# Optimization experiments

Measured on AMD Instinct MI355X. Metric: run time of the kernel, lower is better.

Reference implementation:

```python
import jax, jax.numpy as jnp
import numpy as np

E = 500000
NODE_DIM = 128
EDGE_DIM = 64
OUT_DIM = 128
LN_EPS = 1e-5  # torch nn.LayerNorm default


def setup_inputs() -> dict:
    key = jax.random.key(0)
    ks = jax.random.split(key, 8)
    in_dim = NODE_DIM + EDGE_DIM
    # kaiming-uniform-ish init scale like torch Linear default
    b1 = 1.0 / np.sqrt(in_dim)
    b2 = 1.0 / np.sqrt(OUT_DIM)
    return {
        "source_features": jax.random.normal(ks[0], (E, NODE_DIM), dtype=jnp.float32),
        "edge_features": jax.random.normal(ks[1], (E, EDGE_DIM), dtype=jnp.float32),
        "W1": jax.random.uniform(ks[2], (in_dim, OUT_DIM), jnp.float32, -b1, b1),
        "b1": jax.random.uniform(ks[3], (OUT_DIM,), jnp.float32, -b1, b1),
        "ln_gamma": jnp.ones((OUT_DIM,), jnp.float32),
        "ln_beta": jnp.zeros((OUT_DIM,), jnp.float32),
        "W2": jax.random.uniform(ks[4], (OUT_DIM, OUT_DIM), jnp.float32, -b2, b2),
        "b2": jax.random.uniform(ks[5], (OUT_DIM,), jnp.float32, -b2, b2),
    }


def reference(source_features, edge_features, W1, b1, ln_gamma, ln_beta, W2, b2):
    # Concat source-node and edge features: (E, node_dim + edge_dim)
    x = jnp.concatenate([source_features, edge_features], axis=-1)
    # Linear 1: (E, out_dim)
    h = x @ W1 + b1
    # LayerNorm over last dim (eps matches torch default)
    mu = jnp.mean(h, axis=-1, keepdims=True)
    var = jnp.mean(jnp.square(h - mu), axis=-1, keepdims=True)
    h = (h - mu) * jax.lax.rsqrt(var + LN_EPS) * ln_gamma + ln_beta
    # SiLU -> Linear 2 -> SiLU
    h = jax.nn.silu(h)
    h = h @ W2 + b2
    return jax.nn.silu(h)
```

## Files before the change

### kernel.cpp

```cpp
#include <hip/hip_runtime.h>
#include <stdint.h>

#define E_TOTAL   500000
#define NODE_DIM  128
#define EDGE_DIM  64
#define IN_DIM    192
#define OUT_DIM_  128
#define LN_EPS    1e-5f
#define NTILES    ((E_TOTAL + 63) / 64)

typedef __attribute__((ext_vector_type(8))) short  short8;
typedef __attribute__((ext_vector_type(4))) float  floatx4;
typedef __attribute__((ext_vector_type(4))) unsigned int uintx4;

union Frag { short8 s; uintx4 u; };

__device__ __forceinline__ unsigned int cvtpk(float a, float b) {
    unsigned int r;
    asm("v_cvt_pk_bf16_f32 %0, %1, %2" : "=v"(r) : "v"(a), "v"(b));
    return r;
}
__device__ __forceinline__ unsigned short f2bf1(float a) {
    unsigned int r;
    asm("v_cvt_pk_bf16_f32 %0, %1, %1" : "=v"(r) : "v"(a));
    return (unsigned short)r;
}
__device__ __forceinline__ float fexp2(float x) {
    float r; asm("v_exp_f32 %0, %1" : "=v"(r) : "v"(x)); return r;
}
__device__ __forceinline__ float frcp(float x) {
    float r; asm("v_rcp_f32 %0, %1" : "=v"(r) : "v"(x)); return r;
}
__device__ __forceinline__ float frsq(float x) {
    float r; asm("v_rsq_f32 %0, %1" : "=v"(r) : "v"(x)); return r;
}
__device__ __forceinline__ float silu(float y) {
    return y * frcp(1.0f + fexp2(y * -1.44269504f));
}

__launch_bounds__(256, 2)
__global__ void edge_mlp_kernel(
    const float* __restrict__ src,
    const float* __restrict__ edg,
    const float* __restrict__ W1,
    const float* __restrict__ b1,
    const float* __restrict__ gam,
    const float* __restrict__ bet,
    const float* __restrict__ W2,
    const float* __restrict__ b2,
    float* __restrict__ out)
{
    __shared__ uintx4 w1f[48 * 64];
    __shared__ __align__(16) float ws[4][1088];
    __shared__ float pl[512];

    const int tid  = threadIdx.x;
    const int lane = tid & 63;
    const int wave = tid >> 6;
    const int quad = lane >> 4;
    const int l15  = lane & 15;

    #pragma unroll
    for (int i = 0; i < 12; ++i) {
        int f = wave + 4 * i;
        int s = f >> 3, t = f & 7;
        const float* wp = W1 + (size_t)(s * 32 + quad * 8) * OUT_DIM_ + t * 16 + l15;
        uintx4 v;
        v.x = cvtpk(wp[0],            wp[OUT_DIM_]);
        v.y = cvtpk(wp[2 * OUT_DIM_], wp[3 * OUT_DIM_]);
        v.z = cvtpk(wp[4 * OUT_DIM_], wp[5 * OUT_DIM_]);
        v.w = cvtpk(wp[6 * OUT_DIM_], wp[7 * OUT_DIM_]);
        w1f[f * 64 + lane] = v;
    }
    pl[tid]       = (tid < 128) ? b1[tid]  : gam[tid - 128];
    pl[256 + tid] = (tid < 128) ? bet[tid] : b2[tid - 128];

    Frag w2r[32];
    #pragma unroll
    for (int f = 0; f < 32; ++f) {
        int s = f >> 3, t = f & 7;
        const float* wp = W2 + (size_t)(s * 32 + quad * 8) * OUT_DIM_ + t * 16 + l15;
        w2r[f].u.x = cvtpk(wp[0],            wp[OUT_DIM_]);
        w2r[f].u.y = cvtpk(wp[2 * OUT_DIM_], wp[3 * OUT_DIM_]);
        w2r[f].u.z = cvtpk(wp[4 * OUT_DIM_], wp[5 * OUT_DIM_]);
        w2r[f].u.w = cvtpk(wp[6 * OUT_DIM_], wp[7 * OUT_DIM_]);
    }
    __syncthreads();

    unsigned short* hst = (unsigned short*)&ws[wave][0];
    float*          ost = &ws[wave][0];

    int tile = blockIdx.x;
    floatx4 nx[12];
    {
        int r = tile * 64 + wave * 16 + l15;
        int rc = r < E_TOTAL ? r : (E_TOTAL - 1);
        const float* sp = src + (size_t)rc * NODE_DIM + quad * 8;
        const float* ep = edg + (size_t)rc * EDGE_DIM + quad * 8;
        #pragma unroll
        for (int s = 0; s < 4; ++s) {
            nx[2 * s]     = *(const floatx4*)(sp + s * 32);
            nx[2 * s + 1] = *(const floatx4*)(sp + s * 32 + 4);
        }
        #pragma unroll
        for (int s = 0; s < 2; ++s) {
            nx[8 + 2 * s] = *(const floatx4*)(ep + s * 32);
            nx[9 + 2 * s] = *(const floatx4*)(ep + s * 32 + 4);
        }
    }

    for (; tile < NTILES; tile += gridDim.x) {
        const int rbase = tile * 64 + wave * 16;

        floatx4 acc[8];
        #pragma unroll
        for (int t = 0; t < 8; ++t) {
            float bb = pl[t * 16 + l15];
            acc[t] = (floatx4)(bb);
        }

        #pragma unroll
        for (int s = 0; s < 6; ++s) {
            floatx4 x0 = nx[2 * s];
            floatx4 x1 = nx[2 * s + 1];
            Frag a;
            a.u.x = cvtpk(x0.x, x0.y);
            a.u.y = cvtpk(x0.z, x0.w);
            a.u.z = cvtpk(x1.x, x1.y);
            a.u.w = cvtpk(x1.z, x1.w);
            #pragma unroll
            for (int t = 0; t < 8; ++t) {
                Frag w; w.u = w1f[(s * 8 + t) * 64 + lane];
                acc[t] = __builtin_amdgcn_mfma_f32_16x16x32_bf16(a.s, w.s, acc[t], 0, 0, 0);
            }
        }

        {
            int tn = tile + gridDim.x;
            if (tn < NTILES) {
                int r = tn * 64 + wave * 16 + l15;
                int rc = r < E_TOTAL ? r : (E_TOTAL - 1);
                const float* sp = src + (size_t)rc * NODE_DIM + quad * 8;
                const float* ep = edg + (size_t)rc * EDGE_DIM + quad * 8;
                #pragma unroll
                for (int s = 0; s < 4; ++s) {
                    nx[2 * s]     = *(const floatx4*)(sp + s * 32);
                    nx[2 * s + 1] = *(const floatx4*)(sp + s * 32 + 4);
                }
                #pragma unroll
                for (int s = 0; s < 2; ++s) {
                    nx[8 + 2 * s] = *(const floatx4*)(ep + s * 32);
                    nx[9 + 2 * s] = *(const floatx4*)(ep + s * 32 + 4);
                }
            }
        }

        float S1[4] = {0, 0, 0, 0}, S2[4] = {0, 0, 0, 0};
        #pragma unroll
        for (int t = 0; t < 8; ++t) {
            #pragma unroll
            for (int j = 0; j < 4; ++j) {
                float h = acc[t][j];
                S1[j] += h;
                S2[j] += h * h;
            }
        }
        #pragma unroll
        for (int m = 1; m < 16; m <<= 1) {
            #pragma unroll
            for (int j = 0; j < 4; ++j) {
                S1[j] += __shfl_xor(S1[j], m, 64);
                S2[j] += __shfl_xor(S2[j], m, 64);
            }
        }
        float mu[4], rs[4];
        #pragma unroll
        for (int j = 0; j < 4; ++j) {
            mu[j] = S1[j] * (1.0f / 128.0f);
            float var = S2[j] * (1.0f / 128.0f) - mu[j] * mu[j];
            rs[j] = frsq(var + LN_EPS);
        }

        #pragma unroll
        for (int t = 0; t < 8; ++t) {
            float g  = pl[128 + t * 16 + l15];
            float bt = pl[256 + t * 16 + l15];
            #pragma unroll
            for (int j = 0; j < 4; ++j) {
                float gs  = rs[j] * g;
                float off = __builtin_fmaf(-mu[j], gs, bt);
                float y   = __builtin_fmaf(acc[t][j], gs, off);
                hst[(quad * 4 + j) * 136 + t * 16 + l15] = f2bf1(silu(y));
            }
        }

        #pragma unroll
        for (int t = 0; t < 8; ++t) {
            float bb2 = pl[384 + t * 16 + l15];
            acc[t] = (floatx4)(bb2);
        }
        #pragma unroll
        for (int s2 = 0; s2 < 4; ++s2) {
            Frag a2;
            a2.u = *(const uintx4*)&hst[l15 * 136 + s2 * 32 + quad * 8];
            #pragma unroll
            for (int t = 0; t < 8; ++t) {
                acc[t] = __builtin_amdgcn_mfma_f32_16x16x32_bf16(a2.s, w2r[s2 * 8 + t].s, acc[t], 0, 0, 0);
            }
        }

        #pragma unroll
        for (int p = 0; p < 2; ++p) {
            #pragma unroll
            for (int t = 0; t < 8; ++t) {
                #pragma unroll
                for (int jj = 0; jj < 2; ++jj) {
                    float y = acc[t][2 * p + jj];
                    ost[(quad * 2 + jj) * 136 + t * 16 + l15] = silu(y);
                }
            }
            {
                int a = lane >> 3;
                int b = lane & 7;
                int grow = rbase + (a >> 1) * 4 + 2 * p + (a & 1);
                if (grow < E_TOTAL) {
                    const float* rp = ost + a * 136 + b * 4;
                    float* op = out + (size_t)grow * OUT_DIM_ + b * 4;
                    #pragma unroll
                    for (int c = 0; c < 4; ++c) {
                        *(floatx4*)(op + 32 * c) = *(const floatx4*)(rp + 32 * c);
                    }
                }
            }
        }
    }
}

extern "C" void kernel_launch(void* const* d_in, const int* in_sizes, int n_in,
                              void* d_out, int out_size, void* d_ws, size_t ws_size,
                              hipStream_t stream) {
    const float* src = (const float*)d_in[0];
    const float* edg = (const float*)d_in[1];
    const float* W1  = (const float*)d_in[2];
    const float* b1  = (const float*)d_in[3];
    const float* gam = (const float*)d_in[4];
    const float* bet = (const float*)d_in[5];
    const float* W2  = (const float*)d_in[6];
    const float* b2  = (const float*)d_in[7];
    float* out = (float*)d_out;

    edge_mlp_kernel<<<512, 256, 0, stream>>>(src, edg, W1, b1, gam, bet, W2, b2, out);
}
```

Before: 518.0 us.

## Swap MFMA operands so rows lie in columns, simplifying LayerNorm and staging

Both MFMAs now take the weights as the A operand and the activations as B, so each lane holds four consecutive output features of a single edge row. LayerNorm statistics then need only two cross-quad shuffles per row instead of four shuffle rounds on four values. The normalized hidden values and outputs are written to LDS as 128-bit packed vectors rather than scalar shorts and floats. W2 register fragments are re-permuted to match the new K ordering of the hidden staging, and the output staging uses a 68-float row stride in two 64-column halves, trading a more intricate index mapping for fewer LDS and shuffle instructions.

```diff
diff --git a/kernel.cpp b/kernel.cpp
--- a/kernel.cpp
+++ b/kernel.cpp
@@ -19,11 +19,6 @@
     unsigned int r;
     asm("v_cvt_pk_bf16_f32 %0, %1, %2" : "=v"(r) : "v"(a), "v"(b));
     return r;
-}
-__device__ __forceinline__ unsigned short f2bf1(float a) {
-    unsigned int r;
-    asm("v_cvt_pk_bf16_f32 %0, %1, %1" : "=v"(r) : "v"(a));
-    return (unsigned short)r;
 }
 __device__ __forceinline__ float fexp2(float x) {
     float r; asm("v_exp_f32 %0, %1" : "=v"(r) : "v"(x)); return r;
@@ -59,6 +54,7 @@
     const int wave = tid >> 6;
     const int quad = lane >> 4;
     const int l15  = lane & 15;
+    const int q4   = quad * 4;
 
     #pragma unroll
     for (int i = 0; i < 12; ++i) {
@@ -78,12 +74,12 @@
     Frag w2r[32];
     #pragma unroll
     for (int f = 0; f < 32; ++f) {
-        int s = f >> 3, t = f & 7;
-        const float* wp = W2 + (size_t)(s * 32 + quad * 8) * OUT_DIM_ + t * 16 + l15;
-        w2r[f].u.x = cvtpk(wp[0],            wp[OUT_DIM_]);
-        w2r[f].u.y = cvtpk(wp[2 * OUT_DIM_], wp[3 * OUT_DIM_]);
-        w2r[f].u.z = cvtpk(wp[4 * OUT_DIM_], wp[5 * OUT_DIM_]);
-        w2r[f].u.w = cvtpk(wp[6 * OUT_DIM_], wp[7 * OUT_DIM_]);
+        int s2 = f >> 3, t = f & 7;
+        const float* wp = W2 + (size_t)(32 * quad + 4 * s2) * OUT_DIM_ + t * 16 + l15;
+        w2r[f].u.x = cvtpk(wp[0],              wp[OUT_DIM_]);
+        w2r[f].u.y = cvtpk(wp[2 * OUT_DIM_],   wp[3 * OUT_DIM_]);
+        w2r[f].u.z = cvtpk(wp[16 * OUT_DIM_],  wp[17 * OUT_DIM_]);
+        w2r[f].u.w = cvtpk(wp[18 * OUT_DIM_],  wp[19 * OUT_DIM_]);
     }
     __syncthreads();
 
@@ -114,10 +110,8 @@
 
         floatx4 acc[8];
         #pragma unroll
-        for (int t = 0; t < 8; ++t) {
-            float bb = pl[t * 16 + l15];
-            acc[t] = (floatx4)(bb);
-        }
+        for (int t = 0; t < 8; ++t)
+            acc[t] = *(const floatx4*)&pl[t * 16 + q4];
 
         #pragma unroll
         for (int s = 0; s < 6; ++s) {
@@ -131,7 +125,7 @@
             #pragma unroll
             for (int t = 0; t < 8; ++t) {
                 Frag w; w.u = w1f[(s * 8 + t) * 64 + lane];
-                acc[t] = __builtin_amdgcn_mfma_f32_16x16x32_bf16(a.s, w.s, acc[t], 0, 0, 0);
+                acc[t] = __builtin_amdgcn_mfma_f32_16x16x32_bf16(w.s, a.s, acc[t], 0, 0, 0);
             }
         }
 
@@ -155,81 +149,89 @@
             }
         }
 
-        float S1[4] = {0, 0, 0, 0}, S2[4] = {0, 0, 0, 0};
+        float S1 = 0.0f, S2 = 0.0f;
         #pragma unroll
         for (int t = 0; t < 8; ++t) {
             #pragma unroll
             for (int j = 0; j < 4; ++j) {
                 float h = acc[t][j];
-                S1[j] += h;
-                S2[j] += h * h;
-            }
-        }
-        #pragma unroll
-        for (int m = 1; m < 16; m <<= 1) {
-            #pragma unroll
-            for (int j = 0; j < 4; ++j) {
-                S1[j] += __shfl_xor(S1[j], m, 64);
-                S2[j] += __shfl_xor(S2[j], m, 64);
-            }
-        }
-        float mu[4], rs[4];
-        #pragma unroll
-        for (int j = 0; j < 4; ++j) {
-            mu[j] = S1[j] * (1.0f / 128.0f);
-            float var = S2[j] * (1.0f / 128.0f) - mu[j] * mu[j];
-            rs[j] = frsq(var + LN_EPS);
-        }
-
-        #pragma unroll
-        for (int t = 0; t < 8; ++t) {
-            float g  = pl[128 + t * 16 + l15];
-            float bt = pl[256 + t * 16 + l15];
-            #pragma unroll
-            for (int j = 0; j < 4; ++j) {
-                float gs  = rs[j] * g;
-                float off = __builtin_fmaf(-mu[j], gs, bt);
-                float y   = __builtin_fmaf(acc[t][j], gs, off);
-                hst[(quad * 4 + j) * 136 + t * 16 + l15] = f2bf1(silu(y));
-            }
-        }
-
-        #pragma unroll
-        for (int t = 0; t < 8; ++t) {
-            float bb2 = pl[384 + t * 16 + l15];
-            acc[t] = (floatx4)(bb2);
-        }
+                S1 += h;
+                S2 += h * h;
+            }
+        }
+        S1 += __shfl_xor(S1, 16, 64);
+        S2 += __shfl_xor(S2, 16, 64);
+        S1 += __shfl_xor(S1, 32, 64);
+        S2 += __shfl_xor(S2, 32, 64);
+        float mu = S1 * (1.0f / 128.0f);
+        float var = S2 * (1.0f / 128.0f) - mu * mu;
+        float rs = frsq(var + LN_EPS);
+
+        #pragma unroll
+        for (int u = 0; u < 4; ++u) {
+            uintx4 d;
+            #pragma unroll
+            for (int h2 = 0; h2 < 2; ++h2) {
+                int t = 2 * u + h2;
+                floatx4 g4 = *(const floatx4*)&pl[128 + t * 16 + q4];
+                floatx4 bt4 = *(const floatx4*)&pl[256 + t * 16 + q4];
+                float y0, y1, y2, y3;
+                {
+                    float gs = rs * g4.x;
+                    y0 = silu(__builtin_fmaf(acc[t][0], gs, __builtin_fmaf(-mu, gs, bt4.x)));
+                }
+                {
+                    float gs = rs * g4.y;
+                    y1 = silu(__builtin_fmaf(acc[t][1], gs, __builtin_fmaf(-mu, gs, bt4.y)));
+                }
+                {
+                    float gs = rs * g4.z;
+                    y2 = silu(__builtin_fmaf(acc[t][2], gs, __builtin_fmaf(-mu, gs, bt4.z)));
+                }
+                {
+                    float gs = rs * g4.w;
+                    y3 = silu(__builtin_fmaf(acc[t][3], gs, __builtin_fmaf(-mu, gs, bt4.w)));
+                }
+                if (h2 == 0) { d.x = cvtpk(y0, y1); d.y = cvtpk(y2, y3); }
+                else         { d.z = cvtpk(y0, y1); d.w = cvtpk(y2, y3); }
+            }
+            *(uintx4*)&hst[l15 * 136 + quad * 32 + u * 8] = d;
+        }
+
+        #pragma unroll
+        for (int t = 0; t < 8; ++t)
+            acc[t] = *(const floatx4*)&pl[384 + t * 16 + q4];
+
         #pragma unroll
         for (int s2 = 0; s2 < 4; ++s2) {
-            Frag a2;
-            a2.u = *(const uintx4*)&hst[l15 * 136 + s2 * 32 + quad * 8];
+            Frag hf;
+            hf.u = *(const uintx4*)&hst[l15 * 136 + s2 * 32 + quad * 8];
             #pragma unroll
             for (int t = 0; t < 8; ++t) {
-                acc[t] = __builtin_amdgcn_mfma_f32_16x16x32_bf16(a2.s, w2r[s2 * 8 + t].s, acc[t], 0, 0, 0);
+                acc[t] = __builtin_amdgcn_mfma_f32_16x16x32_bf16(w2r[s2 * 8 + t].s, hf.s, acc[t], 0, 0, 0);
             }
         }
 
         #pragma unroll
         for (int p = 0; p < 2; ++p) {
             #pragma unroll
-            for (int t = 0; t < 8; ++t) {
-                #pragma unroll
-                for (int jj = 0; jj < 2; ++jj) {
-                    float y = acc[t][2 * p + jj];
-                    ost[(quad * 2 + jj) * 136 + t * 16 + l15] = silu(y);
-                }
-            }
-            {
-                int a = lane >> 3;
-                int b = lane & 7;
-                int grow = rbase + (a >> 1) * 4 + 2 * p + (a & 1);
+            for (int tt = 0; tt < 4; ++tt) {
+                int t = p * 4 + tt;
+                floatx4 y;
+                y.x = silu(acc[t][0]);
+                y.y = silu(acc[t][1]);
+                y.z = silu(acc[t][2]);
+                y.w = silu(acc[t][3]);
+                *(floatx4*)&ost[l15 * 68 + tt * 16 + q4] = y;
+            }
+            #pragma unroll
+            for (int v = 0; v < 4; ++v) {
+                int row = v * 4 + (lane >> 4);
+                int c4  = lane & 15;
+                int grow = rbase + row;
                 if (grow < E_TOTAL) {
-                    const float* rp = ost + a * 136 + b * 4;
-                    float* op = out + (size_t)grow * OUT_DIM_ + b * 4;
-                    #pragma unroll
-                    for (int c = 0; c < 4; ++c) {
-                        *(floatx4*)(op + 32 * c) = *(const floatx4*)(rp + 32 * c);
-                    }
+                    floatx4 val = *(const floatx4*)&ost[row * 68 + c4 * 4];
+                    *(floatx4*)(out + (size_t)grow * OUT_DIM_ + p * 64 + c4 * 4) = val;
                 }
             }
         }
```

Result: no change. 527.3 us (+1.8%).
